# Optimization experiments

Measured on AMD Instinct MI355X. Metric: run time of the kernel, lower is better.

Reference implementation:

```python
import jax, jax.numpy as jnp
import numpy as np

B, N, D, H = 4, 2048, 256, 4
HD = D // H


def _linear(x, W, b):
    return x @ W.T + b


def _rotate_half(x):
    # pairs (x0,x1) -> (-x1, x0)
    x1 = x[..., ::2]
    x2 = x[..., 1::2]
    return jnp.stack((-x2, x1), axis=-1).reshape(x.shape)


def _layernorm(x, g, b, eps=1e-5):
    m = jnp.mean(x, axis=-1, keepdims=True)
    v = jnp.mean((x - m) ** 2, axis=-1, keepdims=True)
    return (x - m) / jnp.sqrt(v + eps) * g + b


def _ffn(x, W1, b1, g, be, W2, b2):
    h = _linear(x, W1, b1)
    h = _layernorm(h, g, be)
    h = jax.nn.gelu(h, approximate=False)
    return _linear(h, W2, b2)


def _self_block(x, enc, Wqkv, bqkv, Wout, bout, W1, b1, g, be, W2, b2):
    Bq, Nq, _ = x.shape
    qkv = _linear(x, Wqkv, bqkv).reshape(Bq, Nq, H, HD, 3).transpose(0, 2, 1, 3, 4)  # [B,H,N,HD,3]
    q, k, v = qkv[..., 0], qkv[..., 1], qkv[..., 2]
    q = q * enc[0] + _rotate_half(q) * enc[1]
    k = k * enc[0] + _rotate_half(k) * enc[1]
    scale = HD ** -0.5
    sim = jnp.einsum('bhid,bhjd->bhij', q, k) * scale
    attn = jax.nn.softmax(sim, axis=-1)
    ctx = jnp.einsum('bhij,bhjd->bhid', attn, v)
    msg = _linear(ctx.transpose(0, 2, 1, 3).reshape(Bq, Nq, D), Wout, bout)
    return x + _ffn(jnp.concatenate([x, msg], axis=-1), W1, b1, g, be, W2, b2)


def _cross_block(x0, x1, Wqk, bqk, Wv, bv, Wo, bo, W1, b1, g, be, W2, b2):
    def heads(t):
        return t.reshape(t.shape[0], t.shape[1], H, HD).transpose(0, 2, 1, 3)  # [B,H,N,HD]
    qk0 = heads(_linear(x0, Wqk, bqk))
    qk1 = heads(_linear(x1, Wqk, bqk))
    v0 = heads(_linear(x0, Wv, bv))
    v1 = heads(_linear(x1, Wv, bv))
    s = (HD ** -0.5) ** 0.5
    qk0 = qk0 * s
    qk1 = qk1 * s
    sim = jnp.einsum('bhid,bhjd->bhij', qk0, qk1)
    attn01 = jax.nn.softmax(sim, axis=-1)   # over j (x1 tokens)
    attn10 = jax.nn.softmax(sim, axis=-2)   # over i (x0 tokens)
    m0 = jnp.einsum('bhij,bhjd->bhid', attn01, v1)
    m1 = jnp.einsum('bhij,bhid->bhjd', attn10, v0)
    def unheads(t):
        return t.transpose(0, 2, 1, 3).reshape(t.shape[0], t.shape[2], D)
    m0 = _linear(unheads(m0), Wo, bo)
    m1 = _linear(unheads(m1), Wo, bo)
    x0 = x0 + _ffn(jnp.concatenate([x0, m0], axis=-1), W1, b1, g, be, W2, b2)
    x1 = x1 + _ffn(jnp.concatenate([x1, m1], axis=-1), W1, b1, g, be, W2, b2)
    return x0, x1


def setup_inputs() -> dict:
    key = jax.random.key(0)
    ks = jax.random.split(key, 32)
    std = 0.05

    def rn(k, shape, s=std):
        return jax.random.normal(k, shape, dtype=jnp.float32) * s

    def enc(k):
        ang = jax.random.uniform(k, (B, 1, N, HD // 2), dtype=jnp.float32) * (2 * np.pi)
        cos = jnp.repeat(jnp.cos(ang), 2, axis=-1)
        sin = jnp.repeat(jnp.sin(ang), 2, axis=-1)
        return jnp.stack([cos, sin], axis=0)  # [2,B,1,N,HD]

    return {
        'desc0': rn(ks[0], (B, N, D), 1.0),
        'desc1': rn(ks[1], (B, N, D), 1.0),
        'enc0': enc(ks[2]),
        'enc1': enc(ks[3]),
        's_Wqkv': rn(ks[4], (3 * D, D)), 's_bqkv': jnp.zeros((3 * D,), jnp.float32),
        's_Wout': rn(ks[5], (D, D)), 's_bout': jnp.zeros((D,), jnp.float32),
        's_W1': rn(ks[6], (2 * D, 2 * D)), 's_b1': jnp.zeros((2 * D,), jnp.float32),
        's_g': jnp.ones((2 * D,), jnp.float32), 's_be': jnp.zeros((2 * D,), jnp.float32),
        's_W2': rn(ks[7], (D, 2 * D)), 's_b2': jnp.zeros((D,), jnp.float32),
        'c_Wqk': rn(ks[8], (D, D)), 'c_bqk': jnp.zeros((D,), jnp.float32),
        'c_Wv': rn(ks[9], (D, D)), 'c_bv': jnp.zeros((D,), jnp.float32),
        'c_Wo': rn(ks[10], (D, D)), 'c_bo': jnp.zeros((D,), jnp.float32),
        'c_W1': rn(ks[11], (2 * D, 2 * D)), 'c_b1': jnp.zeros((2 * D,), jnp.float32),
        'c_g': jnp.ones((2 * D,), jnp.float32), 'c_be': jnp.zeros((2 * D,), jnp.float32),
        'c_W2': rn(ks[12], (D, 2 * D)), 'c_b2': jnp.zeros((D,), jnp.float32),
    }


def reference(desc0, desc1, enc0, enc1,
              s_Wqkv, s_bqkv, s_Wout, s_bout, s_W1, s_b1, s_g, s_be, s_W2, s_b2,
              c_Wqk, c_bqk, c_Wv, c_bv, c_Wo, c_bo, c_W1, c_b1, c_g, c_be, c_W2, c_b2):
    d0 = _self_block(desc0, enc0, s_Wqkv, s_bqkv, s_Wout, s_bout, s_W1, s_b1, s_g, s_be, s_W2, s_b2)
    d1 = _self_block(desc1, enc1, s_Wqkv, s_bqkv, s_Wout, s_bout, s_W1, s_b1, s_g, s_be, s_W2, s_b2)
    return _cross_block(d0, d1, c_Wqk, c_bqk, c_Wv, c_bv, c_Wo, c_bo, c_W1, c_b1, c_g, c_be, c_W2, c_b2)
```

## Files before the change

### kernel.cpp

```cpp
#include <hip/hip_runtime.h>
#include <cstddef>

#define NTOK 2048
#define BDIM 4
#define DIM 256
#define NHEAD 4
#define MROWS 8192
#define M2 16384
#define NMu ((size_t)MROWS * DIM)

typedef unsigned short u16;
typedef __attribute__((ext_vector_type(8))) short short8;
typedef __attribute__((ext_vector_type(4))) float f32x4;

#if __has_builtin(__builtin_amdgcn_exp2f)
#define EXP2(x) __builtin_amdgcn_exp2f(x)
#else
#define EXP2(x) exp2f(x)
#endif

__device__ __forceinline__ u16 f2bf(float x) {
  union { float f; unsigned u; } c; c.f = x;
  unsigned r = c.u + 0x7FFFu + ((c.u >> 16) & 1u);
  return (u16)(r >> 16);
}
__device__ __forceinline__ float bf2f(u16 u) {
  union { unsigned u; float f; } c; c.u = ((unsigned)u) << 16;
  return c.f;
}

__device__ __forceinline__ void glds16(const void* g, void* l) {
  __builtin_amdgcn_global_load_lds(
      (const __attribute__((address_space(1))) unsigned int*)g,
      (__attribute__((address_space(3))) unsigned int*)l, 16, 0, 0);
}

__global__ __launch_bounds__(256) void gemm_bf16_kernel(
    const u16* __restrict__ A, int lda,
    const u16* __restrict__ A2, int lda2, int kSplit,
    const u16* __restrict__ W,
    const float* __restrict__ bias0, const float* __restrict__ bias1,
    int nsplit, float os0, float os1,
    u16* __restrict__ Yb0, int ldy0,
    u16* __restrict__ Yb1, int ldy1,
    int K)
{
  __shared__ u16 As[2 * 4096];
  __shared__ u16 Bs[2 * 4096];
  const int t = threadIdx.x;
  const int m0 = blockIdx.y * 128, n0 = blockIdx.x * 128;
  const int r4 = t >> 2, c8 = (t & 3) * 8;
  const int lane = t & 63, w = t >> 6;
  const int cl = lane & 15, quad = lane >> 4;
  const int wm = (w >> 1) * 64, wn = (w & 1) * 64;

  f32x4 acc[4][4];
#pragma unroll
  for (int i = 0; i < 4; ++i)
#pragma unroll
    for (int j = 0; j < 4; ++j) acc[i][j] = (f32x4){0.f, 0.f, 0.f, 0.f};

  for (int k0 = 0; k0 < K; k0 += 64) {
    const u16* Ab; int la; int kk;
    if (k0 < kSplit) { Ab = A; la = lda; kk = k0; }
    else             { Ab = A2; la = lda2; kk = k0 - kSplit; }
    const u16* ag = Ab + (size_t)(m0 + r4) * la + kk + c8;
    const u16* bg = W + (size_t)(n0 + r4) * K + k0 + c8;
    __syncthreads();
#pragma unroll
    for (int kh = 0; kh < 2; ++kh) {
      glds16(ag + kh * 32, &As[kh * 4096 + t * 8]);
      glds16(ag + (size_t)64 * la + kh * 32, &As[kh * 4096 + 2048 + t * 8]);
      glds16(bg + kh * 32, &Bs[kh * 4096 + t * 8]);
      glds16(bg + (size_t)64 * K + kh * 32, &Bs[kh * 4096 + 2048 + t * 8]);
    }
    __syncthreads();

#pragma unroll
    for (int kh = 0; kh < 2; ++kh) {
      short8 af[4], bfr[4];
#pragma unroll
      for (int i = 0; i < 4; ++i)
        af[i] = *(const short8*)&As[kh * 4096 + (wm + i * 16 + cl) * 32 + quad * 8];
#pragma unroll
      for (int i = 0; i < 4; ++i)
        bfr[i] = *(const short8*)&Bs[kh * 4096 + (wn + i * 16 + cl) * 32 + quad * 8];
#pragma unroll
      for (int mt = 0; mt < 4; ++mt)
#pragma unroll
        for (int nt = 0; nt < 4; ++nt)
          acc[mt][nt] = __builtin_amdgcn_mfma_f32_16x16x32_bf16(
              af[mt], bfr[nt], acc[mt][nt], 0, 0, 0);
    }
  }

#pragma unroll
  for (int mt = 0; mt < 4; ++mt)
#pragma unroll
    for (int nt = 0; nt < 4; ++nt) {
      const int colg = n0 + wn + nt * 16 + cl;
      const bool first = colg < nsplit;
      const int c2 = first ? colg : colg - nsplit;
      const float bs = first ? bias0[c2] : bias1[c2];
      const float os = first ? os0 : os1;
      u16* yb = first ? Yb0 : Yb1;
      const int ly = first ? ldy0 : ldy1;
#pragma unroll
      for (int r = 0; r < 4; ++r) {
        const int rowg = m0 + wm + mt * 16 + quad * 4 + r;
        yb[(size_t)rowg * ly + c2] = f2bf((acc[mt][nt][r] + bs) * os);
      }
    }
}

__global__ __launch_bounds__(256) void gemm64_kernel(
    const u16* __restrict__ A, int lda,
    const u16* __restrict__ W,
    const float* __restrict__ bias,
    const u16* __restrict__ resb, int ldrb,
    float* __restrict__ Yf, int ldyf,
    u16* __restrict__ Yb, int ldyb,
    int K)
{
  __shared__ u16 As[2 * 2048];
  __shared__ u16 Bs[2 * 2048];
  const int t = threadIdx.x;
  const int m0 = blockIdx.y * 64, n0 = blockIdx.x * 64;
  const int r8 = t >> 2, c8 = (t & 3) * 8;
  const int lane = t & 63, w = t >> 6;
  const int cl = lane & 15, quad = lane >> 4;
  const int wm = (w >> 1) * 32, wn = (w & 1) * 32;

  f32x4 acc[2][2];
#pragma unroll
  for (int i = 0; i < 2; ++i)
#pragma unroll
    for (int j = 0; j < 2; ++j) acc[i][j] = (f32x4){0.f, 0.f, 0.f, 0.f};

  for (int k0 = 0; k0 < K; k0 += 64) {
    const u16* ag = A + (size_t)(m0 + r8) * lda + k0 + c8;
    const u16* bg = W + (size_t)(n0 + r8) * K + k0 + c8;
    __syncthreads();
#pragma unroll
    for (int kh = 0; kh < 2; ++kh) {
      glds16(ag + kh * 32, &As[kh * 2048 + t * 8]);
      glds16(bg + kh * 32, &Bs[kh * 2048 + t * 8]);
    }
    __syncthreads();

#pragma unroll
    for (int kh = 0; kh < 2; ++kh) {
      short8 af[2], bfr[2];
#pragma unroll
      for (int i = 0; i < 2; ++i)
        af[i] = *(const short8*)&As[kh * 2048 + (wm + i * 16 + cl) * 32 + quad * 8];
#pragma unroll
      for (int j = 0; j < 2; ++j)
        bfr[j] = *(const short8*)&Bs[kh * 2048 + (wn + j * 16 + cl) * 32 + quad * 8];
#pragma unroll
      for (int mt = 0; mt < 2; ++mt)
#pragma unroll
        for (int nt = 0; nt < 2; ++nt)
          acc[mt][nt] = __builtin_amdgcn_mfma_f32_16x16x32_bf16(
              af[mt], bfr[nt], acc[mt][nt], 0, 0, 0);
    }
  }

#pragma unroll
  for (int mt = 0; mt < 2; ++mt)
#pragma unroll
    for (int nt = 0; nt < 2; ++nt) {
      const int colg = n0 + wn + nt * 16 + cl;
      const float bs = bias[colg];
#pragma unroll
      for (int r = 0; r < 4; ++r) {
        const int rowg = m0 + wm + mt * 16 + quad * 4 + r;
        float v = acc[mt][nt][r] + bs;
        if (resb) v += bf2f(resb[(size_t)rowg * ldrb + colg]);
        if (Yf) Yf[(size_t)rowg * ldyf + colg] = v;
        if (Yb) Yb[(size_t)rowg * ldyb + colg] = f2bf(v);
      }
    }
}

__global__ __launch_bounds__(256) void wfuse_kernel(
    const float* __restrict__ W1, const float* __restrict__ Wo,
    const float* __restrict__ b1, const float* __restrict__ bo,
    const float* __restrict__ cW1, const float* __restrict__ cWo,
    const float* __restrict__ cb1, const float* __restrict__ cbo,
    u16* __restrict__ W1f, u16* __restrict__ cW1f,
    float* __restrict__ b1f, float* __restrict__ cb1f)
{
  const int n = blockIdx.x, sel = blockIdx.y;
  const float* Ws = sel ? cW1 : W1;
  const float* Wos = sel ? cWo : Wo;
  u16* out = sel ? cW1f : W1f;
  __shared__ float rowh[256];
  const int t = threadIdx.x;
  rowh[t] = Ws[(size_t)n * 512 + 256 + t];
  out[(size_t)n * 512 + t] = f2bf(Ws[(size_t)n * 512 + t]);
  __syncthreads();
  float acc = 0.f;
  for (int m = 0; m < 256; ++m) acc += rowh[m] * Wos[(size_t)m * 256 + t];
  out[(size_t)n * 512 + 256 + t] = f2bf(acc);
  if (t == 0) {
    const float* bos = sel ? cbo : bo;
    const float* b1s = sel ? cb1 : b1;
    float a = b1s[n];
    for (int m = 0; m < 256; ++m) a += rowh[m] * bos[m];
    (sel ? cb1f : b1f)[n] = a;
  }
}

__global__ __launch_bounds__(256) void rope_repack_kernel(
    const u16* __restrict__ qkv, const float* __restrict__ enc0,
    const float* __restrict__ enc1,
    u16* __restrict__ Q, u16* __restrict__ K, u16* __restrict__ V)
{
  const int idx = blockIdx.x * blockDim.x + threadIdx.x;
  const int i = idx & 31;
  const int h = (idx >> 5) & 3;
  const int m = idx >> 7;
  const int half = m >> 13;
  const int lm = m & (MROWS - 1);
  const float* enc = half ? enc1 : enc0;
  const u16* src = qkv + (size_t)m * 768 + h * 192 + i * 6;
  const unsigned a0 = *(const unsigned*)(src);
  const unsigned a1 = *(const unsigned*)(src + 2);
  const unsigned a2 = *(const unsigned*)(src + 4);
  const float q0 = bf2f((u16)a0), k0 = bf2f((u16)(a0 >> 16));
  const float v0 = bf2f((u16)a1), q1 = bf2f((u16)(a1 >> 16));
  const float k1 = bf2f((u16)a2), v1 = bf2f((u16)(a2 >> 16));
  const float c = enc[(size_t)lm * 64 + 2 * i];
  const float s = enc[(size_t)MROWS * 64 + (size_t)lm * 64 + 2 * i];
  const float QSC = 0.18033688011112042f;
  const size_t o = (size_t)m * 256 + h * 64 + 2 * i;
  *(unsigned*)(Q + o) = (unsigned)f2bf((q0 * c - q1 * s) * QSC) |
                        ((unsigned)f2bf((q1 * c + q0 * s) * QSC) << 16);
  *(unsigned*)(K + o) = (unsigned)f2bf(k0 * c - k1 * s) |
                        ((unsigned)f2bf(k1 * c + k0 * s) << 16);
  *(unsigned*)(V + o) = (unsigned)f2bf(v0) | ((unsigned)f2bf(v1) << 16);
}

__global__ __launch_bounds__(256) void transpose_v_kernel(
    const u16* __restrict__ in, u16* __restrict__ out)
{
  __shared__ u16 Tl[64][72];
  const int bz = blockIdx.z, h = blockIdx.y;
  const int n0 = blockIdx.x * 64;
  const int t = threadIdx.x;
  {
    const int row = t >> 2, c16 = (t & 3) * 16;
    const u16* src = in + (size_t)(bz * NTOK + n0 + row) * 256 + h * 64 + c16;
    *(uint4*)&Tl[row][c16] = *(const uint4*)src;
    *(uint4*)&Tl[row][c16 + 8] = *(const uint4*)(src + 8);
  }
  __syncthreads();
  const int d = t >> 2, qr = t & 3;
  union { u16 u[16]; uint4 v[2]; } pk;
#pragma unroll
  for (int j = 0; j < 16; ++j) pk.u[j] = Tl[qr * 16 + j][d];
  u16* dst = out + ((size_t)((bz * NHEAD + h) * 64 + d)) * NTOK + n0 + qr * 16;
  *(uint4*)dst = pk.v[0];
  *(uint4*)(dst + 8) = pk.v[1];
}

__global__ __launch_bounds__(256, 2) void attn5_kernel(
    const u16* __restrict__ Qb, const u16* __restrict__ Kb,
    const u16* __restrict__ Vtb, u16* __restrict__ Ou, int cross)
{
  __shared__ u16 Ks[2][64 * 64];
  __shared__ u16 Vs[2][64 * 64];
  __shared__ u16 Ps[4][32 * 64];

  const int hw = blockIdx.x;
  const int li = hw >> 3;
  const int y  = (hw & 7) * 4 + (li >> 4);
  const int n0 = (li & 15) * 128;

  const int h2 = y >> 4, b = (y >> 2) & 3, h = y & 3;
  const int kh = cross ? (1 - h2) : h2;
  const int qrowbase = (h2 * 4 + b) * NTOK;
  const int krowbase = (kh * 4 + b) * NTOK;
  const int vz = kh * 4 + b;
  const int t = threadIdx.x, lane = t & 63, w = t >> 6;
  const int cl = lane & 15, quad = lane >> 4;
  const int q0 = w * 32;
  const int fsw = (cl & 7) << 4;

  short8 bq[2][2];
#pragma unroll
  for (int c = 0; c < 2; ++c) {
    const u16* qsrc = Qb + (size_t)(qrowbase + n0 + q0 + c * 16 + cl) * 256 +
                      h * 64 + quad * 8;
    bq[c][0] = *(const short8*)qsrc;
    bq[c][1] = *(const short8*)(qsrc + 32);
  }

  float l_r[2] = {0.f, 0.f};
  f32x4 o[2][4];
#pragma unroll
  for (int c = 0; c < 2; ++c)
#pragma unroll
    for (int i = 0; i < 4; ++i) o[c][i] = (f32x4){0.f, 0.f, 0.f, 0.f};

  const int srow = t >> 2;
  const int scb = (t & 3) * 32;
  const int ssw = (srow & 7) << 4;
  const u16* Kg = Kb + (size_t)(krowbase + srow) * 256 + h * 64 + (t & 3) * 16;
  const u16* Vg = Vtb + ((size_t)(vz * NHEAD + h) * 64 + srow) * NTOK + (t & 3) * 16;

  uint4 ka0 = *(const uint4*)Kg, ka1 = *(const uint4*)(Kg + 8);
  uint4 va0 = *(const uint4*)Vg, va1 = *(const uint4*)(Vg + 8);
  {
    char* kd = (char*)&Ks[0][srow * 64];
    *(uint4*)(kd + (scb ^ ssw)) = ka0;
    *(uint4*)(kd + ((scb + 16) ^ ssw)) = ka1;
    char* vd = (char*)&Vs[0][srow * 64];
    *(uint4*)(vd + (scb ^ ssw)) = va0;
    *(uint4*)(vd + ((scb + 16) ^ ssw)) = va1;
  }
  Kg += 64 * 256; Vg += 64;
  ka0 = *(const uint4*)Kg; ka1 = *(const uint4*)(Kg + 8);
  va0 = *(const uint4*)Vg; va1 = *(const uint4*)(Vg + 8);
  __syncthreads();

  for (int tile = 0; tile < 32; ++tile) {
    const int cur = tile & 1, nxt = cur ^ 1;

    f32x4 sf[2][4];
    __builtin_amdgcn_s_setprio(1);
#pragma unroll
    for (int kb = 0; kb < 4; ++kb) {
      const char* kr = (const char*)&Ks[cur][(kb * 16 + cl) * 64];
      short8 ak0 = *(const short8*)(kr + ((quad * 16) ^ fsw));
      short8 ak1 = *(const short8*)(kr + ((quad * 16 + 64) ^ fsw));
#pragma unroll
      for (int c = 0; c < 2; ++c) {
        f32x4 acc = (f32x4){0.f, 0.f, 0.f, 0.f};
        acc = __builtin_amdgcn_mfma_f32_16x16x32_bf16(ak0, bq[c][0], acc, 0, 0, 0);
        acc = __builtin_amdgcn_mfma_f32_16x16x32_bf16(ak1, bq[c][1], acc, 0, 0, 0);
        sf[c][kb] = acc;
      }
    }
    __builtin_amdgcn_s_setprio(0);

    if (tile < 31) {
      char* kd = (char*)&Ks[nxt][srow * 64];
      *(uint4*)(kd + (scb ^ ssw)) = ka0;
      *(uint4*)(kd + ((scb + 16) ^ ssw)) = ka1;
      if (tile < 30) {
        Kg += 64 * 256;
        ka0 = *(const uint4*)Kg; ka1 = *(const uint4*)(Kg + 8);
      }
    }

#pragma unroll
    for (int c = 0; c < 2; ++c) {
      float rs = 0.f;
#pragma unroll
      for (int kb = 0; kb < 4; ++kb)
#pragma unroll
        for (int r = 0; r < 4; ++r) {
          const float p = EXP2(sf[c][kb][r]);
          sf[c][kb][r] = p; rs += p;
        }
      rs += __shfl_xor(rs, 16);
      rs += __shfl_xor(rs, 32);
      l_r[c] += rs;
      char* pd = (char*)&Ps[w][(c * 16 + cl) * 64];
#pragma unroll
      for (int kb = 0; kb < 4; ++kb) {
        unsigned d0 = __builtin_amdgcn_perm(__float_as_uint(sf[c][kb][1]),
                                            __float_as_uint(sf[c][kb][0]), 0x07060302u);
        unsigned d1 = __builtin_amdgcn_perm(__float_as_uint(sf[c][kb][3]),
                                            __float_as_uint(sf[c][kb][2]), 0x07060302u);
        uint2 pk; pk.x = d0; pk.y = d1;
        *(uint2*)(pd + ((kb * 32 + quad * 8) ^ fsw)) = pk;
      }
    }

    short8 bp[2][2];
#pragma unroll
    for (int c = 0; c < 2; ++c) {
      const char* pr = (const char*)&Ps[w][(c * 16 + cl) * 64];
      bp[c][0] = *(const short8*)(pr + ((quad * 16) ^ fsw));
      bp[c][1] = *(const short8*)(pr + ((quad * 16 + 64) ^ fsw));
    }
    __builtin_amdgcn_s_setprio(1);
#pragma unroll
    for (int db = 0; db < 4; ++db) {
      const char* vr = (const char*)&Vs[cur][(db * 16 + cl) * 64];
      short8 av0 = *(const short8*)(vr + ((quad * 16) ^ fsw));
      short8 av1 = *(const short8*)(vr + ((quad * 16 + 64) ^ fsw));
#pragma unroll
      for (int c = 0; c < 2; ++c) {
        o[c][db] = __builtin_amdgcn_mfma_f32_16x16x32_bf16(av0, bp[c][0], o[c][db], 0, 0, 0);
        o[c][db] = __builtin_amdgcn_mfma_f32_16x16x32_bf16(av1, bp[c][1], o[c][db], 0, 0, 0);
      }
    }
    __builtin_amdgcn_s_setprio(0);

    if (tile < 31) {
      char* vd = (char*)&Vs[nxt][srow * 64];
      *(uint4*)(vd + (scb ^ ssw)) = va0;
      *(uint4*)(vd + ((scb + 16) ^ ssw)) = va1;
      if (tile < 30) {
        Vg += 64;
        va0 = *(const uint4*)Vg; va1 = *(const uint4*)(Vg + 8);
      }
    }
    __syncthreads();
  }

#pragma unroll
  for (int c = 0; c < 2; ++c) {
    const float inv = 1.f / l_r[c];
    const size_t rowo = (size_t)(qrowbase + n0 + q0 + c * 16 + cl) * 256 + h * 64;
#pragma unroll
    for (int db = 0; db < 4; ++db) {
      ushort4 st;
      st.x = f2bf(o[c][db][0] * inv); st.y = f2bf(o[c][db][1] * inv);
      st.z = f2bf(o[c][db][2] * inv); st.w = f2bf(o[c][db][3] * inv);
      *(ushort4*)(Ou + rowo + db * 16 + quad * 4) = st;
    }
  }
}

__global__ __launch_bounds__(256) void ln_gelu_kernel(
    const u16* __restrict__ Hm, const float* __restrict__ g,
    const float* __restrict__ be, u16* __restrict__ out)
{
  const int rowi = blockIdx.x * 4 + (threadIdx.x >> 6);
  const int lane = threadIdx.x & 63;
  const u16* row = Hm + (size_t)rowi * 512 + lane * 8;
  u16* orow = out + (size_t)rowi * 512 + lane * 8;
  uint4 raw = *(const uint4*)row;
  float x[8];
  const unsigned* rw = (const unsigned*)&raw;
#pragma unroll
  for (int i = 0; i < 4; ++i) {
    x[2 * i]     = bf2f((u16)rw[i]);
    x[2 * i + 1] = bf2f((u16)(rw[i] >> 16));
  }
  float s = 0.f;
#pragma unroll
  for (int i = 0; i < 8; ++i) s += x[i];
#pragma unroll
  for (int off = 32; off; off >>= 1) s += __shfl_xor(s, off);
  const float mean = s * (1.f / 512.f);
  float s2 = 0.f;
#pragma unroll
  for (int i = 0; i < 8; ++i) { const float d = x[i] - mean; s2 += d * d; }
#pragma unroll
  for (int off = 32; off; off >>= 1) s2 += __shfl_xor(s2, off);
  const float rstd = rsqrtf(s2 * (1.f / 512.f) + 1e-5f);
  unsigned ov[4];
#pragma unroll
  for (int i = 0; i < 4; ++i) {
    const int c = lane * 8 + 2 * i;
    const float y0 = (x[2 * i] - mean) * rstd * g[c] + be[c];
    const float y1 = (x[2 * i + 1] - mean) * rstd * g[c + 1] + be[c + 1];
    const float g0 = 0.5f * y0 * (1.f + erff(y0 * 0.70710678118654752f));
    const float g1 = 0.5f * y1 * (1.f + erff(y1 * 0.70710678118654752f));
    ov[i] = (unsigned)f2bf(g0) | ((unsigned)f2bf(g1) << 16);
  }
  *(uint4*)orow = *(uint4*)ov;
}

__global__ __launch_bounds__(256) void pack_all_kernel(
    const float* w0, const float* w1, const float* w2, const float* w3,
    const float* w4, const float* d0, const float* d1,
    u16* __restrict__ wb, u16* __restrict__ descb)
{
  const size_t idx4 = ((size_t)blockIdx.x * 256 + threadIdx.x) * 4;
  const float* src; u16* dst; size_t off;
  if (idx4 < 589824) {
    off = idx4; dst = wb + idx4;
    if      (idx4 < 196608) { src = w0; }
    else if (idx4 < 327680) { src = w1; off -= 196608; }
    else if (idx4 < 393216) { src = w2; off -= 327680; }
    else if (idx4 < 458752) { src = w3; off -= 393216; }
    else                    { src = w4; off -= 458752; }
  } else {
    size_t o = idx4 - 589824;
    dst = descb + o;
    if (o < NMu) { src = d0; off = o; }
    else         { src = d1; off = o - NMu; }
  }
  float4 v = *(const float4*)(src + off);
  ushort4 ov;
  ov.x = f2bf(v.x); ov.y = f2bf(v.y); ov.z = f2bf(v.z); ov.w = f2bf(v.w);
  *(ushort4*)dst = ov;
}

extern "C" void kernel_launch(void* const* d_in, const int* in_sizes, int n_in,
                              void* d_out, int out_size, void* d_ws, size_t ws_size,
                              hipStream_t stream) {
  const float* desc0  = (const float*)d_in[0];
  const float* desc1  = (const float*)d_in[1];
  const float* enc0   = (const float*)d_in[2];
  const float* enc1   = (const float*)d_in[3];
  const float* s_Wqkv = (const float*)d_in[4];
  const float* s_bqkv = (const float*)d_in[5];
  const float* s_Wout = (const float*)d_in[6];
  const float* s_bout = (const float*)d_in[7];
  const float* s_W1   = (const float*)d_in[8];
  const float* s_b1   = (const float*)d_in[9];
  const float* s_g    = (const float*)d_in[10];
  const float* s_be   = (const float*)d_in[11];
  const float* s_W2   = (const float*)d_in[12];
  const float* s_b2   = (const float*)d_in[13];
  const float* c_Wqk  = (const float*)d_in[14];
  const float* c_bqk  = (const float*)d_in[15];
  const float* c_Wv   = (const float*)d_in[16];
  const float* c_bv   = (const float*)d_in[17];
  const float* c_Wo   = (const float*)d_in[18];
  const float* c_bo   = (const float*)d_in[19];
  const float* c_W1   = (const float*)d_in[20];
  const float* c_b1   = (const float*)d_in[21];
  const float* c_g    = (const float*)d_in[22];
  const float* c_be   = (const float*)d_in[23];
  const float* c_W2   = (const float*)d_in[24];
  const float* c_b2   = (const float*)d_in[25];

  u16* U = (u16*)d_ws;
  u16* descb = U + 0 * NMu;
  u16* qkvb  = U + 2 * NMu;
  u16* ctxb  = U + 2 * NMu;
  u16* Qu    = U + 8 * NMu;
  u16* Ku    = U + 10 * NMu;
  u16* Vu    = U + 12 * NMu;
  u16* Vt    = U + 14 * NMu;
  u16* hbufb = U + 12 * NMu;
  u16* hb2   = U + 16 * NMu;
  float* b1f = (float*)(U + 20 * NMu);
  float* cb1f = b1f + 512;
  u16* s_b   = U + 21 * NMu;
  u16* wb    = U + 23 * NMu;

  u16* Wqkvb = wb;
  u16* W2b   = wb + 196608;
  u16* cQKVb = wb + 327680;
  u16* cW2b  = wb + 458752;
  u16* W1f   = wb + 589824;
  u16* cW1f  = wb + 851968;

  float* outf = (float*)d_out;

  const dim3 tv_grid(NTOK / 64, NHEAD, 8);
  const int rope_blocks = (M2 * 128) / 256;
  const int lng_blocks  = M2 / 4;
  const float csc = 0.42466090014400953f;

  hipLaunchKernelGGL(pack_all_kernel, dim3(4672), dim3(256), 0, stream,
                     s_Wqkv, s_W2, c_Wqk, c_Wv, c_W2, desc0, desc1, wb, descb);
  hipLaunchKernelGGL(wfuse_kernel, dim3(512, 2), dim3(256), 0, stream,
                     s_W1, s_Wout, s_b1, s_bout, c_W1, c_Wo, c_b1, c_bo,
                     W1f, cW1f, b1f, cb1f);

  hipLaunchKernelGGL(gemm_bf16_kernel, dim3(6, 128), dim3(256), 0, stream,
                     descb, 256, (const u16*)nullptr, 0, 1 << 30, Wqkvb,
                     s_bqkv, (const float*)nullptr, 1 << 30, 1.f, 1.f,
                     qkvb, 768, (u16*)nullptr, 0, 256);
  hipLaunchKernelGGL(rope_repack_kernel, dim3(rope_blocks), dim3(256), 0, stream,
                     qkvb, enc0, enc1, Qu, Ku, Vu);
  hipLaunchKernelGGL(transpose_v_kernel, tv_grid, dim3(256), 0, stream, Vu, Vt);
  hipLaunchKernelGGL(attn5_kernel, dim3(512), dim3(256), 0, stream,
                     Qu, Ku, Vt, ctxb, 0);
  hipLaunchKernelGGL(gemm_bf16_kernel, dim3(4, 128), dim3(256), 0, stream,
                     descb, 256, ctxb, 256, 256, W1f,
                     b1f, (const float*)nullptr, 1 << 30, 1.f, 1.f,
                     hbufb, 512, (u16*)nullptr, 0, 512);
  hipLaunchKernelGGL(ln_gelu_kernel, dim3(lng_blocks), dim3(256), 0, stream,
                     hbufb, s_g, s_be, hb2);
  hipLaunchKernelGGL(gemm64_kernel, dim3(4, 256), dim3(256), 0, stream,
                     hb2, 512, W2b, s_b2, descb, 256,
                     (float*)nullptr, 0, s_b, 256, 512);

  u16* qkb = Qu;
  u16* vb  = Ku;
  hipLaunchKernelGGL(gemm_bf16_kernel, dim3(4, 128), dim3(256), 0, stream,
                     s_b, 256, (const u16*)nullptr, 0, 1 << 30, cQKVb,
                     c_bqk, c_bv, 256, csc, 1.f,
                     qkb, 256, vb, 256, 256);
  hipLaunchKernelGGL(transpose_v_kernel, tv_grid, dim3(256), 0, stream, vb, Vt);
  hipLaunchKernelGGL(attn5_kernel, dim3(512), dim3(256), 0, stream,
                     qkb, qkb, Vt, ctxb, 1);
  hipLaunchKernelGGL(gemm_bf16_kernel, dim3(4, 128), dim3(256), 0, stream,
                     s_b, 256, ctxb, 256, 256, cW1f,
                     cb1f, (const float*)nullptr, 1 << 30, 1.f, 1.f,
                     hbufb, 512, (u16*)nullptr, 0, 512);
  hipLaunchKernelGGL(ln_gelu_kernel, dim3(lng_blocks), dim3(256), 0, stream,
                     hbufb, c_g, c_be, hb2);
  hipLaunchKernelGGL(gemm64_kernel, dim3(4, 256), dim3(256), 0, stream,
                     hb2, 512, cW2b, c_b2, s_b, 256,
                     outf, 256, (u16*)nullptr, 0, 512);
}
```

Measured before the change: 372.9 us.

## Unify GEMMs: stage weights in LDS, stream A from global, XCD-aware block mapping

Replaces the two GEMM kernels with one templated kernel. Each block stages a 256-wide K chunk of the weight tile in LDS, while each wave reads its A fragments straight from global memory into registers. Blocks are remapped so consecutive row tiles land on the same XCD, and the residual add and fp32 output move into the shared epilogue. This cuts LDS traffic and barriers for A and improves L2 locality. The cost is exposed, partly uncoalesced global-load latency on A with no prefetching.

```diff
diff --git a/kernel.cpp b/kernel.cpp
--- a/kernel.cpp
+++ b/kernel.cpp
@@ -35,58 +35,71 @@
       (__attribute__((address_space(3))) unsigned int*)l, 16, 0, 0);
 }
 
-__global__ __launch_bounds__(256) void gemm_bf16_kernel(
+template<int NC>
+__global__ __launch_bounds__(256) void gemm_ws_kernel(
     const u16* __restrict__ A, int lda,
     const u16* __restrict__ A2, int lda2, int kSplit,
     const u16* __restrict__ W,
     const float* __restrict__ bias0, const float* __restrict__ bias1,
     int nsplit, float os0, float os1,
+    const u16* __restrict__ resb, int ldrb,
+    float* __restrict__ Yf, int ldyf,
     u16* __restrict__ Yb0, int ldy0,
     u16* __restrict__ Yb1, int ldy1,
-    int K)
-{
-  __shared__ u16 As[2 * 4096];
-  __shared__ u16 Bs[2 * 4096];
+    int K, int Nx)
+{
+  constexpr int MF = (NC == 128) ? 4 : 2;
+  __shared__ u16 Bs[8 * NC * 32];
+
+  const int gid = blockIdx.x;
+  const int xcd = gid & 7;
+  const int li  = gid >> 3;
+  const int nx  = li >> 4;
+  const int y   = xcd * 16 + (li & 15);
+  const int n0  = nx * NC;
+
   const int t = threadIdx.x;
-  const int m0 = blockIdx.y * 128, n0 = blockIdx.x * 128;
-  const int r4 = t >> 2, c8 = (t & 3) * 8;
   const int lane = t & 63, w = t >> 6;
   const int cl = lane & 15, quad = lane >> 4;
-  const int wm = (w >> 1) * 64, wn = (w & 1) * 64;
-
-  f32x4 acc[4][4];
-#pragma unroll
-  for (int i = 0; i < 4; ++i)
+  const int wm = (NC == 128) ? (w >> 1) * 64 : w * 32;
+  const int wn = (NC == 128) ? (w & 1) * 64 : 0;
+  const int m0 = y * 128 + wm;
+
+  f32x4 acc[MF][4];
+#pragma unroll
+  for (int i = 0; i < MF; ++i)
 #pragma unroll
     for (int j = 0; j < 4; ++j) acc[i][j] = (f32x4){0.f, 0.f, 0.f, 0.f};
 
-  for (int k0 = 0; k0 < K; k0 += 64) {
-    const u16* Ab; int la; int kk;
-    if (k0 < kSplit) { Ab = A; la = lda; kk = k0; }
-    else             { Ab = A2; la = lda2; kk = k0 - kSplit; }
-    const u16* ag = Ab + (size_t)(m0 + r4) * la + kk + c8;
-    const u16* bg = W + (size_t)(n0 + r4) * K + k0 + c8;
+  for (int kc = 0; kc < K; kc += 256) {
     __syncthreads();
 #pragma unroll
-    for (int kh = 0; kh < 2; ++kh) {
-      glds16(ag + kh * 32, &As[kh * 4096 + t * 8]);
-      glds16(ag + (size_t)64 * la + kh * 32, &As[kh * 4096 + 2048 + t * 8]);
-      glds16(bg + kh * 32, &Bs[kh * 4096 + t * 8]);
-      glds16(bg + (size_t)64 * K + kh * 32, &Bs[kh * 4096 + 2048 + t * 8]);
+    for (int ks = 0; ks < 8; ++ks) {
+      glds16(W + (size_t)(n0 + (t >> 2)) * K + kc + ks * 32 + (t & 3) * 8,
+             &Bs[ks * (NC * 32) + t * 8]);
+      if constexpr (NC == 128)
+        glds16(W + (size_t)(n0 + 64 + (t >> 2)) * K + kc + ks * 32 + (t & 3) * 8,
+               &Bs[ks * (NC * 32) + 2048 + t * 8]);
     }
     __syncthreads();
 
-#pragma unroll
-    for (int kh = 0; kh < 2; ++kh) {
-      short8 af[4], bfr[4];
-#pragma unroll
-      for (int i = 0; i < 4; ++i)
-        af[i] = *(const short8*)&As[kh * 4096 + (wm + i * 16 + cl) * 32 + quad * 8];
-#pragma unroll
-      for (int i = 0; i < 4; ++i)
-        bfr[i] = *(const short8*)&Bs[kh * 4096 + (wn + i * 16 + cl) * 32 + quad * 8];
-#pragma unroll
-      for (int mt = 0; mt < 4; ++mt)
+    const u16* Ap = (kc < kSplit) ? A : A2;
+    const int  la = (kc < kSplit) ? lda : lda2;
+    const int  kb = (kc < kSplit) ? kc : kc - kSplit;
+    const u16* ag = Ap + (size_t)(m0 + cl) * la + kb + quad * 8;
+
+#pragma unroll
+    for (int ks = 0; ks < 8; ++ks) {
+      short8 af[MF];
+#pragma unroll
+      for (int mt = 0; mt < MF; ++mt)
+        af[mt] = *(const short8*)(ag + (size_t)mt * 16 * la + ks * 32);
+      short8 bfr[4];
+#pragma unroll
+      for (int nt = 0; nt < 4; ++nt)
+        bfr[nt] = *(const short8*)&Bs[ks * (NC * 32) + (wn + nt * 16 + cl) * 32 + quad * 8];
+#pragma unroll
+      for (int mt = 0; mt < MF; ++mt)
 #pragma unroll
         for (int nt = 0; nt < 4; ++nt)
           acc[mt][nt] = __builtin_amdgcn_mfma_f32_16x16x32_bf16(
@@ -95,7 +108,7 @@
   }
 
 #pragma unroll
-  for (int mt = 0; mt < 4; ++mt)
+  for (int mt = 0; mt < MF; ++mt)
 #pragma unroll
     for (int nt = 0; nt < 4; ++nt) {
       const int colg = n0 + wn + nt * 16 + cl;
@@ -107,78 +120,11 @@
       const int ly = first ? ldy0 : ldy1;
 #pragma unroll
       for (int r = 0; r < 4; ++r) {
-        const int rowg = m0 + wm + mt * 16 + quad * 4 + r;
-        yb[(size_t)rowg * ly + c2] = f2bf((acc[mt][nt][r] + bs) * os);
-      }
-    }
-}
-
-__global__ __launch_bounds__(256) void gemm64_kernel(
-    const u16* __restrict__ A, int lda,
-    const u16* __restrict__ W,
-    const float* __restrict__ bias,
-    const u16* __restrict__ resb, int ldrb,
-    float* __restrict__ Yf, int ldyf,
-    u16* __restrict__ Yb, int ldyb,
-    int K)
-{
-  __shared__ u16 As[2 * 2048];
-  __shared__ u16 Bs[2 * 2048];
-  const int t = threadIdx.x;
-  const int m0 = blockIdx.y * 64, n0 = blockIdx.x * 64;
-  const int r8 = t >> 2, c8 = (t & 3) * 8;
-  const int lane = t & 63, w = t >> 6;
-  const int cl = lane & 15, quad = lane >> 4;
-  const int wm = (w >> 1) * 32, wn = (w & 1) * 32;
-
-  f32x4 acc[2][2];
-#pragma unroll
-  for (int i = 0; i < 2; ++i)
-#pragma unroll
-    for (int j = 0; j < 2; ++j) acc[i][j] = (f32x4){0.f, 0.f, 0.f, 0.f};
-
-  for (int k0 = 0; k0 < K; k0 += 64) {
-    const u16* ag = A + (size_t)(m0 + r8) * lda + k0 + c8;
-    const u16* bg = W + (size_t)(n0 + r8) * K + k0 + c8;
-    __syncthreads();
-#pragma unroll
-    for (int kh = 0; kh < 2; ++kh) {
-      glds16(ag + kh * 32, &As[kh * 2048 + t * 8]);
-      glds16(bg + kh * 32, &Bs[kh * 2048 + t * 8]);
-    }
-    __syncthreads();
-
-#pragma unroll
-    for (int kh = 0; kh < 2; ++kh) {
-      short8 af[2], bfr[2];
-#pragma unroll
-      for (int i = 0; i < 2; ++i)
-        af[i] = *(const short8*)&As[kh * 2048 + (wm + i * 16 + cl) * 32 + quad * 8];
-#pragma unroll
-      for (int j = 0; j < 2; ++j)
-        bfr[j] = *(const short8*)&Bs[kh * 2048 + (wn + j * 16 + cl) * 32 + quad * 8];
-#pragma unroll
-      for (int mt = 0; mt < 2; ++mt)
-#pragma unroll
-        for (int nt = 0; nt < 2; ++nt)
-          acc[mt][nt] = __builtin_amdgcn_mfma_f32_16x16x32_bf16(
-              af[mt], bfr[nt], acc[mt][nt], 0, 0, 0);
-    }
-  }
-
-#pragma unroll
-  for (int mt = 0; mt < 2; ++mt)
-#pragma unroll
-    for (int nt = 0; nt < 2; ++nt) {
-      const int colg = n0 + wn + nt * 16 + cl;
-      const float bs = bias[colg];
-#pragma unroll
-      for (int r = 0; r < 4; ++r) {
-        const int rowg = m0 + wm + mt * 16 + quad * 4 + r;
-        float v = acc[mt][nt][r] + bs;
+        const int rowg = m0 + mt * 16 + quad * 4 + r;
+        float v = (acc[mt][nt][r] + bs) * os;
         if (resb) v += bf2f(resb[(size_t)rowg * ldrb + colg]);
         if (Yf) Yf[(size_t)rowg * ldyf + colg] = v;
-        if (Yb) Yb[(size_t)rowg * ldyb + colg] = f2bf(v);
+        if (yb) yb[(size_t)rowg * ly + c2] = f2bf(v);
       }
     }
 }
@@ -552,6 +498,9 @@
   const int rope_blocks = (M2 * 128) / 256;
   const int lng_blocks  = M2 / 4;
   const float csc = 0.42466090014400953f;
+  const int BIG = 1 << 30;
+  const u16* NU = (const u16*)nullptr;
+  const float* NF = (const float*)nullptr;
 
   hipLaunchKernelGGL(pack_all_kernel, dim3(4672), dim3(256), 0, stream,
                      s_Wqkv, s_W2, c_Wqk, c_Wv, c_W2, desc0, desc1, wb, descb);
@@ -559,41 +508,49 @@
                      s_W1, s_Wout, s_b1, s_bout, c_W1, c_Wo, c_b1, c_bo,
                      W1f, cW1f, b1f, cb1f);
 
-  hipLaunchKernelGGL(gemm_bf16_kernel, dim3(6, 128), dim3(256), 0, stream,
-                     descb, 256, (const u16*)nullptr, 0, 1 << 30, Wqkvb,
-                     s_bqkv, (const float*)nullptr, 1 << 30, 1.f, 1.f,
-                     qkvb, 768, (u16*)nullptr, 0, 256);
+  hipLaunchKernelGGL((gemm_ws_kernel<128>), dim3(6 * 128), dim3(256), 0, stream,
+                     descb, 256, NU, 0, BIG, Wqkvb,
+                     s_bqkv, NF, BIG, 1.f, 1.f,
+                     NU, 0, (float*)nullptr, 0,
+                     qkvb, 768, (u16*)nullptr, 0, 256, 6);
   hipLaunchKernelGGL(rope_repack_kernel, dim3(rope_blocks), dim3(256), 0, stream,
                      qkvb, enc0, enc1, Qu, Ku, Vu);
   hipLaunchKernelGGL(transpose_v_kernel, tv_grid, dim3(256), 0, stream, Vu, Vt);
   hipLaunchKernelGGL(attn5_kernel, dim3(512), dim3(256), 0, stream,
                      Qu, Ku, Vt, ctxb, 0);
-  hipLaunchKernelGGL(gemm_bf16_kernel, dim3(4, 128), dim3(256), 0, stream,
+  hipLaunchKernelGGL((gemm_ws_kernel<128>), dim3(4 * 128), dim3(256), 0, stream,
                      descb, 256, ctxb, 256, 256, W1f,
-                     b1f, (const float*)nullptr, 1 << 30, 1.f, 1.f,
-                     hbufb, 512, (u16*)nullptr, 0, 512);
+                     b1f, NF, BIG, 1.f, 1.f,
+                     NU, 0, (float*)nullptr, 0,
+                     hbufb, 512, (u16*)nullptr, 0, 512, 4);
   hipLaunchKernelGGL(ln_gelu_kernel, dim3(lng_blocks), dim3(256), 0, stream,
                      hbufb, s_g, s_be, hb2);
-  hipLaunchKernelGGL(gemm64_kernel, dim3(4, 256), dim3(256), 0, stream,
-                     hb2, 512, W2b, s_b2, descb, 256,
-                     (float*)nullptr, 0, s_b, 256, 512);
+  hipLaunchKernelGGL((gemm_ws_kernel<64>), dim3(4 * 128), dim3(256), 0, stream,
+                     hb2, 512, NU, 0, BIG, W2b,
+                     s_b2, NF, BIG, 1.f, 1.f,
+                     descb, 256, (float*)nullptr, 0,
+                     s_b, 256, (u16*)nullptr, 0, 512, 4);
 
   u16* qkb = Qu;
   u16* vb  = Ku;
-  hipLaunchKernelGGL(gemm_bf16_kernel, dim3(4, 128), dim3(256), 0, stream,
-                     s_b, 256, (const u16*)nullptr, 0, 1 << 30, cQKVb,
+  hipLaunchKernelGGL((gemm_ws_kernel<128>), dim3(4 * 128), dim3(256), 0, stream,
+                     s_b, 256, NU, 0, BIG, cQKVb,
                      c_bqk, c_bv, 256, csc, 1.f,
-                     qkb, 256, vb, 256, 256);
+                     NU, 0, (float*)nullptr, 0,
+                     qkb, 256, vb, 256, 256, 4);
   hipLaunchKernelGGL(transpose_v_kernel, tv_grid, dim3(256), 0, stream, vb, Vt);
   hipLaunchKernelGGL(attn5_kernel, dim3(512), dim3(256), 0, stream,
                      qkb, qkb, Vt, ctxb, 1);
-  hipLaunchKernelGGL(gemm_bf16_kernel, dim3(4, 128), dim3(256), 0, stream,
+  hipLaunchKernelGGL((gemm_ws_kernel<128>), dim3(4 * 128), dim3(256), 0, stream,
                      s_b, 256, ctxb, 256, 256, cW1f,
-                     cb1f, (const float*)nullptr, 1 << 30, 1.f, 1.f,
-                     hbufb, 512, (u16*)nullptr, 0, 512);
+                     cb1f, NF, BIG, 1.f, 1.f,
+                     NU, 0, (float*)nullptr, 0,
+                     hbufb, 512, (u16*)nullptr, 0, 512, 4);
   hipLaunchKernelGGL(ln_gelu_kernel, dim3(lng_blocks), dim3(256), 0, stream,
                      hbufb, c_g, c_be, hb2);
-  hipLaunchKernelGGL(gemm64_kernel, dim3(4, 256), dim3(256), 0, stream,
-                     hb2, 512, cW2b, c_b2, s_b, 256,
-                     outf, 256, (u16*)nullptr, 0, 512);
-}
+  hipLaunchKernelGGL((gemm_ws_kernel<64>), dim3(4 * 128), dim3(256), 0, stream,
+                     hb2, 512, NU, 0, BIG, cW2b,
+                     c_b2, NF, BIG, 1.f, 1.f,
+                     s_b, 256, outf, 256,
+                     (u16*)nullptr, 0, (u16*)nullptr, 0, 512, 4);
+}
```

Result: slower. 403.1 us (+8.1%).

## Load attention K/V fragments directly from global memory, dropping LDS staging and barriers

Applied to the files above, without the earlier changes.

The attention kernel no longer stages K and V tiles in shared memory with double buffering and a per-tile barrier. Each wave now loads its MFMA operand fragments straight from global memory into registers, prefetching the next K tile during softmax. This removes LDS writes and reads and the block-wide sync. In exchange, each of the four waves re-reads K/V from cache, and V loads are exposed at the start of each tile. The launch bound no longer requests two blocks per CU.

```diff
diff --git a/kernel.cpp b/kernel.cpp
--- a/kernel.cpp
+++ b/kernel.cpp
@@ -265,12 +265,10 @@
   *(uint4*)(dst + 8) = pk.v[1];
 }
 
-__global__ __launch_bounds__(256, 2) void attn5_kernel(
+__global__ __launch_bounds__(256) void attn6_kernel(
     const u16* __restrict__ Qb, const u16* __restrict__ Kb,
     const u16* __restrict__ Vtb, u16* __restrict__ Ou, int cross)
 {
-  __shared__ u16 Ks[2][64 * 64];
-  __shared__ u16 Vs[2][64 * 64];
   __shared__ u16 Ps[4][32 * 64];
 
   const int hw = blockIdx.x;
@@ -304,54 +302,49 @@
 #pragma unroll
     for (int i = 0; i < 4; ++i) o[c][i] = (f32x4){0.f, 0.f, 0.f, 0.f};
 
-  const int srow = t >> 2;
-  const int scb = (t & 3) * 32;
-  const int ssw = (srow & 7) << 4;
-  const u16* Kg = Kb + (size_t)(krowbase + srow) * 256 + h * 64 + (t & 3) * 16;
-  const u16* Vg = Vtb + ((size_t)(vz * NHEAD + h) * 64 + srow) * NTOK + (t & 3) * 16;
-
-  uint4 ka0 = *(const uint4*)Kg, ka1 = *(const uint4*)(Kg + 8);
-  uint4 va0 = *(const uint4*)Vg, va1 = *(const uint4*)(Vg + 8);
-  {
-    char* kd = (char*)&Ks[0][srow * 64];
-    *(uint4*)(kd + (scb ^ ssw)) = ka0;
-    *(uint4*)(kd + ((scb + 16) ^ ssw)) = ka1;
-    char* vd = (char*)&Vs[0][srow * 64];
-    *(uint4*)(vd + (scb ^ ssw)) = va0;
-    *(uint4*)(vd + ((scb + 16) ^ ssw)) = va1;
-  }
-  Kg += 64 * 256; Vg += 64;
-  ka0 = *(const uint4*)Kg; ka1 = *(const uint4*)(Kg + 8);
-  va0 = *(const uint4*)Vg; va1 = *(const uint4*)(Vg + 8);
-  __syncthreads();
+  const u16* Kp = Kb + (size_t)(krowbase + cl) * 256 + h * 64 + quad * 8;
+  const u16* Vp = Vtb + ((size_t)(vz * NHEAD + h) * 64 + cl) * NTOK + quad * 8;
+
+  short8 kf[4][2], vf[4][2];
+#pragma unroll
+  for (int kb = 0; kb < 4; ++kb) {
+    const u16* ks = Kp + (size_t)(kb * 16) * 256;
+    kf[kb][0] = *(const short8*)ks;
+    kf[kb][1] = *(const short8*)(ks + 32);
+  }
 
   for (int tile = 0; tile < 32; ++tile) {
-    const int cur = tile & 1, nxt = cur ^ 1;
+    {
+      const u16* vs = Vp + tile * 64;
+#pragma unroll
+      for (int db = 0; db < 4; ++db) {
+        const u16* vr = vs + (size_t)(db * 16) * NTOK;
+        vf[db][0] = *(const short8*)vr;
+        vf[db][1] = *(const short8*)(vr + 32);
+      }
+    }
 
     f32x4 sf[2][4];
     __builtin_amdgcn_s_setprio(1);
 #pragma unroll
     for (int kb = 0; kb < 4; ++kb) {
-      const char* kr = (const char*)&Ks[cur][(kb * 16 + cl) * 64];
-      short8 ak0 = *(const short8*)(kr + ((quad * 16) ^ fsw));
-      short8 ak1 = *(const short8*)(kr + ((quad * 16 + 64) ^ fsw));
 #pragma unroll
       for (int c = 0; c < 2; ++c) {
         f32x4 acc = (f32x4){0.f, 0.f, 0.f, 0.f};
-        acc = __builtin_amdgcn_mfma_f32_16x16x32_bf16(ak0, bq[c][0], acc, 0, 0, 0);
-        acc = __builtin_amdgcn_mfma_f32_16x16x32_bf16(ak1, bq[c][1], acc, 0, 0, 0);
+        acc = __builtin_amdgcn_mfma_f32_16x16x32_bf16(kf[kb][0], bq[c][0], acc, 0, 0, 0);
+        acc = __builtin_amdgcn_mfma_f32_16x16x32_bf16(kf[kb][1], bq[c][1], acc, 0, 0, 0);
         sf[c][kb] = acc;
       }
     }
     __builtin_amdgcn_s_setprio(0);
 
     if (tile < 31) {
-      char* kd = (char*)&Ks[nxt][srow * 64];
-      *(uint4*)(kd + (scb ^ ssw)) = ka0;
-      *(uint4*)(kd + ((scb + 16) ^ ssw)) = ka1;
-      if (tile < 30) {
-        Kg += 64 * 256;
-        ka0 = *(const uint4*)Kg; ka1 = *(const uint4*)(Kg + 8);
+      const u16* ks0 = Kp + (size_t)(tile + 1) * 64 * 256;
+#pragma unroll
+      for (int kb = 0; kb < 4; ++kb) {
+        const u16* ks = ks0 + (size_t)(kb * 16) * 256;
+        kf[kb][0] = *(const short8*)ks;
+        kf[kb][1] = *(const short8*)(ks + 32);
       }
     }
 
@@ -390,27 +383,13 @@
     __builtin_amdgcn_s_setprio(1);
 #pragma unroll
     for (int db = 0; db < 4; ++db) {
-      const char* vr = (const char*)&Vs[cur][(db * 16 + cl) * 64];
-      short8 av0 = *(const short8*)(vr + ((quad * 16) ^ fsw));
-      short8 av1 = *(const short8*)(vr + ((quad * 16 + 64) ^ fsw));
 #pragma unroll
       for (int c = 0; c < 2; ++c) {
-        o[c][db] = __builtin_amdgcn_mfma_f32_16x16x32_bf16(av0, bp[c][0], o[c][db], 0, 0, 0);
-        o[c][db] = __builtin_amdgcn_mfma_f32_16x16x32_bf16(av1, bp[c][1], o[c][db], 0, 0, 0);
+        o[c][db] = __builtin_amdgcn_mfma_f32_16x16x32_bf16(vf[db][0], bp[c][0], o[c][db], 0, 0, 0);
+        o[c][db] = __builtin_amdgcn_mfma_f32_16x16x32_bf16(vf[db][1], bp[c][1], o[c][db], 0, 0, 0);
       }
     }
     __builtin_amdgcn_s_setprio(0);
-
-    if (tile < 31) {
-      char* vd = (char*)&Vs[nxt][srow * 64];
-      *(uint4*)(vd + (scb ^ ssw)) = va0;
-      *(uint4*)(vd + ((scb + 16) ^ ssw)) = va1;
-      if (tile < 30) {
-        Vg += 64;
-        va0 = *(const uint4*)Vg; va1 = *(const uint4*)(Vg + 8);
-      }
-    }
-    __syncthreads();
   }
 
 #pragma unroll
@@ -566,7 +545,7 @@
   hipLaunchKernelGGL(rope_repack_kernel, dim3(rope_blocks), dim3(256), 0, stream,
                      qkvb, enc0, enc1, Qu, Ku, Vu);
   hipLaunchKernelGGL(transpose_v_kernel, tv_grid, dim3(256), 0, stream, Vu, Vt);
-  hipLaunchKernelGGL(attn5_kernel, dim3(512), dim3(256), 0, stream,
+  hipLaunchKernelGGL(attn6_kernel, dim3(512), dim3(256), 0, stream,
                      Qu, Ku, Vt, ctxb, 0);
   hipLaunchKernelGGL(gemm_bf16_kernel, dim3(4, 128), dim3(256), 0, stream,
                      descb, 256, ctxb, 256, 256, W1f,
@@ -585,7 +564,7 @@
                      c_bqk, c_bv, 256, csc, 1.f,
                      qkb, 256, vb, 256, 256);
   hipLaunchKernelGGL(transpose_v_kernel, tv_grid, dim3(256), 0, stream, vb, Vt);
-  hipLaunchKernelGGL(attn5_kernel, dim3(512), dim3(256), 0, stream,
+  hipLaunchKernelGGL(attn6_kernel, dim3(512), dim3(256), 0, stream,
                      qkb, qkb, Vt, ctxb, 1);
   hipLaunchKernelGGL(gemm_bf16_kernel, dim3(4, 128), dim3(256), 0, stream,
                      s_b, 256, ctxb, 256, 256, cW1f,
```

New measurement: 514.3 us. +37.9%, slower.

## Split attention KV range in two with combine kernel; XCD-aware GEMM tile mapping

Applied to the files above, without the earlier changes.

Attention now processes half the key/value sequence per block, doubling the grid, and writes unnormalized partial outputs and row sums that a new combine kernel sums and normalizes. This targets low occupancy from the 512-block attention grid. GEMM kernels switch to a 1D grid remapped so consecutive row tiles land on the same XCD, aiming for better L2 reuse. It adds partial-output traffic and an extra launch per attention.

```diff
diff --git a/kernel.cpp b/kernel.cpp
--- a/kernel.cpp
+++ b/kernel.cpp
@@ -43,12 +43,19 @@
     int nsplit, float os0, float os1,
     u16* __restrict__ Yb0, int ldy0,
     u16* __restrict__ Yb1, int ldy1,
-    int K)
+    int K, int mshift)
 {
   __shared__ u16 As[2 * 4096];
   __shared__ u16 Bs[2 * 4096];
   const int t = threadIdx.x;
-  const int m0 = blockIdx.y * 128, n0 = blockIdx.x * 128;
+
+  const int gid = blockIdx.x;
+  const int xcd = gid & 7;
+  const int li  = gid >> 3;
+  const int mloc = li & ((1 << mshift) - 1);
+  const int nx   = li >> mshift;
+  const int m0 = ((xcd << mshift) | mloc) * 128, n0 = nx * 128;
+
   const int r4 = t >> 2, c8 = (t & 3) * 8;
   const int lane = t & 63, w = t >> 6;
   const int cl = lane & 15, quad = lane >> 4;
@@ -120,12 +127,19 @@
     const u16* __restrict__ resb, int ldrb,
     float* __restrict__ Yf, int ldyf,
     u16* __restrict__ Yb, int ldyb,
-    int K)
+    int K, int mshift)
 {
   __shared__ u16 As[2 * 2048];
   __shared__ u16 Bs[2 * 2048];
   const int t = threadIdx.x;
-  const int m0 = blockIdx.y * 64, n0 = blockIdx.x * 64;
+
+  const int gid = blockIdx.x;
+  const int xcd = gid & 7;
+  const int li  = gid >> 3;
+  const int mloc = li & ((1 << mshift) - 1);
+  const int nx   = li >> mshift;
+  const int m0 = ((xcd << mshift) | mloc) * 64, n0 = nx * 64;
+
   const int r8 = t >> 2, c8 = (t & 3) * 8;
   const int lane = t & 63, w = t >> 6;
   const int cl = lane & 15, quad = lane >> 4;
@@ -265,23 +279,27 @@
   *(uint4*)(dst + 8) = pk.v[1];
 }
 
-__global__ __launch_bounds__(256, 2) void attn5_kernel(
+__global__ __launch_bounds__(256, 2) void attn7_kernel(
     const u16* __restrict__ Qb, const u16* __restrict__ Kb,
-    const u16* __restrict__ Vtb, u16* __restrict__ Ou, int cross)
+    const u16* __restrict__ Vtb,
+    u16* __restrict__ Po, float* __restrict__ Pl, int cross)
 {
   __shared__ u16 Ks[2][64 * 64];
   __shared__ u16 Vs[2][64 * 64];
   __shared__ u16 Ps[4][32 * 64];
 
   const int hw = blockIdx.x;
-  const int li = hw >> 3;
-  const int y  = (hw & 7) * 4 + (li >> 4);
-  const int n0 = (li & 15) * 128;
+  const int xcd = hw & 7;
+  const int li  = hw >> 3;
+  const int y   = xcd * 4 + (li >> 5);
+  const int r5  = li & 31;
+  const int z   = r5 >> 4;
+  const int n0  = (r5 & 15) * 128;
 
   const int h2 = y >> 4, b = (y >> 2) & 3, h = y & 3;
   const int kh = cross ? (1 - h2) : h2;
   const int qrowbase = (h2 * 4 + b) * NTOK;
-  const int krowbase = (kh * 4 + b) * NTOK;
+  const int krowbase = (kh * 4 + b) * NTOK + z * 1024;
   const int vz = kh * 4 + b;
   const int t = threadIdx.x, lane = t & 63, w = t >> 6;
   const int cl = lane & 15, quad = lane >> 4;
@@ -308,7 +326,8 @@
   const int scb = (t & 3) * 32;
   const int ssw = (srow & 7) << 4;
   const u16* Kg = Kb + (size_t)(krowbase + srow) * 256 + h * 64 + (t & 3) * 16;
-  const u16* Vg = Vtb + ((size_t)(vz * NHEAD + h) * 64 + srow) * NTOK + (t & 3) * 16;
+  const u16* Vg = Vtb + ((size_t)(vz * NHEAD + h) * 64 + srow) * NTOK +
+                  z * 1024 + (t & 3) * 16;
 
   uint4 ka0 = *(const uint4*)Kg, ka1 = *(const uint4*)(Kg + 8);
   uint4 va0 = *(const uint4*)Vg, va1 = *(const uint4*)(Vg + 8);
@@ -325,7 +344,7 @@
   va0 = *(const uint4*)Vg; va1 = *(const uint4*)(Vg + 8);
   __syncthreads();
 
-  for (int tile = 0; tile < 32; ++tile) {
+  for (int tile = 0; tile < 16; ++tile) {
     const int cur = tile & 1, nxt = cur ^ 1;
 
     f32x4 sf[2][4];
@@ -345,11 +364,11 @@
     }
     __builtin_amdgcn_s_setprio(0);
 
-    if (tile < 31) {
+    if (tile < 15) {
       char* kd = (char*)&Ks[nxt][srow * 64];
       *(uint4*)(kd + (scb ^ ssw)) = ka0;
       *(uint4*)(kd + ((scb + 16) ^ ssw)) = ka1;
-      if (tile < 30) {
+      if (tile < 14) {
         Kg += 64 * 256;
         ka0 = *(const uint4*)Kg; ka1 = *(const uint4*)(Kg + 8);
       }
@@ -401,11 +420,11 @@
     }
     __builtin_amdgcn_s_setprio(0);
 
-    if (tile < 31) {
+    if (tile < 15) {
       char* vd = (char*)&Vs[nxt][srow * 64];
       *(uint4*)(vd + (scb ^ ssw)) = va0;
       *(uint4*)(vd + ((scb + 16) ^ ssw)) = va1;
-      if (tile < 30) {
+      if (tile < 14) {
         Vg += 64;
         va0 = *(const uint4*)Vg; va1 = *(const uint4*)(Vg + 8);
       }
@@ -415,16 +434,32 @@
 
 #pragma unroll
   for (int c = 0; c < 2; ++c) {
-    const float inv = 1.f / l_r[c];
-    const size_t rowo = (size_t)(qrowbase + n0 + q0 + c * 16 + cl) * 256 + h * 64;
+    const int rp = z * 65536 + y * 2048 + n0 + q0 + c * 16 + cl;
 #pragma unroll
     for (int db = 0; db < 4; ++db) {
       ushort4 st;
-      st.x = f2bf(o[c][db][0] * inv); st.y = f2bf(o[c][db][1] * inv);
-      st.z = f2bf(o[c][db][2] * inv); st.w = f2bf(o[c][db][3] * inv);
-      *(ushort4*)(Ou + rowo + db * 16 + quad * 4) = st;
-    }
-  }
+      st.x = f2bf(o[c][db][0]); st.y = f2bf(o[c][db][1]);
+      st.z = f2bf(o[c][db][2]); st.w = f2bf(o[c][db][3]);
+      *(ushort4*)(Po + (size_t)rp * 64 + db * 16 + quad * 4) = st;
+    }
+    if (quad == 0) { Pl[rp] = l_r[c]; }
+  }
+}
+
+__global__ __launch_bounds__(256) void attn_combine_kernel(
+    const u16* __restrict__ Po, const float* __restrict__ Pl,
+    u16* __restrict__ Ou)
+{
+  const int rowi = blockIdx.x * 4 + (threadIdx.x >> 6);
+  const int lane = threadIdx.x & 63;
+  const float l0 = Pl[rowi], l1 = Pl[65536 + rowi];
+  const float inv = 1.f / (l0 + l1);
+  const float o0 = bf2f(Po[(size_t)rowi * 64 + lane]);
+  const float o1 = bf2f(Po[(size_t)65536 * 64 + (size_t)rowi * 64 + lane]);
+  const float val = (o0 + o1) * inv;
+  const int y = rowi >> 11, q = rowi & 2047;
+  const int bz = y >> 2, h = y & 3;
+  Ou[(size_t)(bz * NTOK + q) * 256 + h * 64 + lane] = f2bf(val);
 }
 
 __global__ __launch_bounds__(256) void ln_gelu_kernel(
@@ -533,8 +568,10 @@
   u16* Vu    = U + 12 * NMu;
   u16* Vt    = U + 14 * NMu;
   u16* hbufb = U + 12 * NMu;
+  u16* Po    = U + 16 * NMu;
   u16* hb2   = U + 16 * NMu;
-  float* b1f = (float*)(U + 20 * NMu);
+  float* Pl  = (float*)(U + 20 * NMu);
+  float* b1f = Pl + 2 * 65536;
   float* cb1f = b1f + 512;
   u16* s_b   = U + 21 * NMu;
   u16* wb    = U + 23 * NMu;
@@ -551,6 +588,7 @@
   const dim3 tv_grid(NTOK / 64, NHEAD, 8);
   const int rope_blocks = (M2 * 128) / 256;
   const int lng_blocks  = M2 / 4;
+  const int comb_blocks = 65536 / 4;
   const float csc = 0.42466090014400953f;
 
   hipLaunchKernelGGL(pack_all_kernel, dim3(4672), dim3(256), 0, stream,
@@ -559,41 +597,45 @@
                      s_W1, s_Wout, s_b1, s_bout, c_W1, c_Wo, c_b1, c_bo,
                      W1f, cW1f, b1f, cb1f);
 
-  hipLaunchKernelGGL(gemm_bf16_kernel, dim3(6, 128), dim3(256), 0, stream,
+  hipLaunchKernelGGL(gemm_bf16_kernel, dim3(768), dim3(256), 0, stream,
                      descb, 256, (const u16*)nullptr, 0, 1 << 30, Wqkvb,
                      s_bqkv, (const float*)nullptr, 1 << 30, 1.f, 1.f,
-                     qkvb, 768, (u16*)nullptr, 0, 256);
+                     qkvb, 768, (u16*)nullptr, 0, 256, 4);
   hipLaunchKernelGGL(rope_repack_kernel, dim3(rope_blocks), dim3(256), 0, stream,
                      qkvb, enc0, enc1, Qu, Ku, Vu);
   hipLaunchKernelGGL(transpose_v_kernel, tv_grid, dim3(256), 0, stream, Vu, Vt);
-  hipLaunchKernelGGL(attn5_kernel, dim3(512), dim3(256), 0, stream,
-                     Qu, Ku, Vt, ctxb, 0);
-  hipLaunchKernelGGL(gemm_bf16_kernel, dim3(4, 128), dim3(256), 0, stream,
+  hipLaunchKernelGGL(attn7_kernel, dim3(1024), dim3(256), 0, stream,
+                     Qu, Ku, Vt, Po, Pl, 0);
+  hipLaunchKernelGGL(attn_combine_kernel, dim3(comb_blocks), dim3(256), 0, stream,
+                     Po, Pl, ctxb);
+  hipLaunchKernelGGL(gemm_bf16_kernel, dim3(512), dim3(256), 0, stream,
                      descb, 256, ctxb, 256, 256, W1f,
                      b1f, (const float*)nullptr, 1 << 30, 1.f, 1.f,
-                     hbufb, 512, (u16*)nullptr, 0, 512);
+                     hbufb, 512, (u16*)nullptr, 0, 512, 4);
   hipLaunchKernelGGL(ln_gelu_kernel, dim3(lng_blocks), dim3(256), 0, stream,
                      hbufb, s_g, s_be, hb2);
-  hipLaunchKernelGGL(gemm64_kernel, dim3(4, 256), dim3(256), 0, stream,
+  hipLaunchKernelGGL(gemm64_kernel, dim3(1024), dim3(256), 0, stream,
                      hb2, 512, W2b, s_b2, descb, 256,
-                     (float*)nullptr, 0, s_b, 256, 512);
+                     (float*)nullptr, 0, s_b, 256, 512, 5);
 
   u16* qkb = Qu;
   u16* vb  = Ku;
-  hipLaunchKernelGGL(gemm_bf16_kernel, dim3(4, 128), dim3(256), 0, stream,
+  hipLaunchKernelGGL(gemm_bf16_kernel, dim3(512), dim3(256), 0, stream,
                      s_b, 256, (const u16*)nullptr, 0, 1 << 30, cQKVb,
                      c_bqk, c_bv, 256, csc, 1.f,
-                     qkb, 256, vb, 256, 256);
+                     qkb, 256, vb, 256, 256, 4);
   hipLaunchKernelGGL(transpose_v_kernel, tv_grid, dim3(256), 0, stream, vb, Vt);
-  hipLaunchKernelGGL(attn5_kernel, dim3(512), dim3(256), 0, stream,
-                     qkb, qkb, Vt, ctxb, 1);
-  hipLaunchKernelGGL(gemm_bf16_kernel, dim3(4, 128), dim3(256), 0, stream,
+  hipLaunchKernelGGL(attn7_kernel, dim3(1024), dim3(256), 0, stream,
+                     qkb, qkb, Vt, Po, Pl, 1);
+  hipLaunchKernelGGL(attn_combine_kernel, dim3(comb_blocks), dim3(256), 0, stream,
+                     Po, Pl, ctxb);
+  hipLaunchKernelGGL(gemm_bf16_kernel, dim3(512), dim3(256), 0, stream,
                      s_b, 256, ctxb, 256, 256, cW1f,
                      cb1f, (const float*)nullptr, 1 << 30, 1.f, 1.f,
-                     hbufb, 512, (u16*)nullptr, 0, 512);
+                     hbufb, 512, (u16*)nullptr, 0, 512, 4);
   hipLaunchKernelGGL(ln_gelu_kernel, dim3(lng_blocks), dim3(256), 0, stream,
                      hbufb, c_g, c_be, hb2);
-  hipLaunchKernelGGL(gemm64_kernel, dim3(4, 256), dim3(256), 0, stream,
+  hipLaunchKernelGGL(gemm64_kernel, dim3(1024), dim3(256), 0, stream,
                      hb2, 512, cW2b, c_b2, s_b, 256,
-                     outf, 256, (u16*)nullptr, 0, 512);
-}
+                     outf, 256, (u16*)nullptr, 0, 512, 5);
+}
```

Result: slower. 381.2 us (+2.2%).
